# Optimization experiments

Measured on AMD Instinct MI355X. Metric: run time of the kernel, lower is better.

Reference implementation:

```python
import jax, jax.numpy as jnp
import numpy as np

N, E = 50000, 600000
NODE_DIM, EDGE_DIM, MSG_DIM = 128, 64, 128


def setup_inputs() -> dict:
    key = jax.random.key(0)
    ks = jax.random.split(key, 8)
    s = 0.05
    return {
        "node_features": jax.random.normal(ks[0], (N, NODE_DIM), jnp.float32),
        "edge_features": jax.random.normal(ks[1], (E, EDGE_DIM), jnp.float32),
        "edge_index": jax.random.randint(ks[2], (2, E), 0, N, jnp.int32),
        "We1": jax.random.normal(ks[3], (2 * NODE_DIM + EDGE_DIM, 32), jnp.float32) * s,
        "be1": jnp.zeros((32,), jnp.float32),
        "We2": jax.random.normal(ks[4], (32, MSG_DIM), jnp.float32) * s,
        "be2": jnp.zeros((MSG_DIM,), jnp.float32),
        "Wn1": jax.random.normal(ks[5], (NODE_DIM + MSG_DIM, 64), jnp.float32) * s,
        "bn1": jnp.zeros((64,), jnp.float32),
        "Wn2": jax.random.normal(ks[6], (64, MSG_DIM), jnp.float32) * s,
        "bn2": jnp.zeros((MSG_DIM,), jnp.float32),
    }


def reference(node_features, edge_features, edge_index,
              We1, be1, We2, be2, Wn1, bn1, Wn2, bn2):
    src, dst = edge_index[0], edge_index[1]
    src_f = node_features[src]            # [E, node_dim] gather
    dst_f = node_features[dst]            # [E, node_dim] gather
    # edge message encoder: 2-layer MLP with ReLU
    edge_in = jnp.concatenate([src_f, dst_f, edge_features], axis=1)  # [E, 2*nd+ed]
    h = jax.nn.relu(edge_in @ We1 + be1)
    edge_msg = jax.nn.relu(h @ We2 + be2)  # [E, msg_dim]
    # node message encoder
    node_in = jnp.concatenate([dst_f, edge_msg], axis=1)  # [E, nd+md]
    h2 = jax.nn.relu(node_in @ Wn1 + bn1)
    node_msg = jax.nn.relu(h2 @ Wn2 + bn2)  # [E, msg_dim]
    # scatter-sum over destination nodes (replaces the O(N) python loop)
    agg = jax.ops.segment_sum(node_msg, dst, num_segments=node_features.shape[0])
    return node_features + agg
```

## Files before the change

kernel.cpp:

```cpp
#include <hip/hip_runtime.h>
#include <hip/hip_bf16.h>

constexpr int N_NODES = 50000;
constexpr int N_EDGES = 600000;
constexpr int ND = 128;
constexpr int ED = 64;
constexpr int MD = 128;
constexpr int H1 = 32;
constexpr int H2 = 64;

typedef __attribute__((ext_vector_type(8))) short short8;
typedef __attribute__((ext_vector_type(4))) float f32x4;
typedef __attribute__((ext_vector_type(4))) unsigned int uint32x4;

#define MFMA16(a, b, c) __builtin_amdgcn_mfma_f32_16x16x32_bf16((a), (b), (c), 0, 0, 0)

constexpr int COUNTS_PAD = 53248;
constexpr size_t WS_SLOTREC = 0;
constexpr size_t WS_PRE     = WS_SLOTREC + (size_t)N_EDGES * 16;
constexpr size_t WS_POS     = WS_PRE + (size_t)N_NODES * 128 * 2;
constexpr size_t WS_COUNTS  = WS_POS + (size_t)N_EDGES * 4;
constexpr size_t WS_OFFSETS = WS_COUNTS + (size_t)COUNTS_PAD * 4;
constexpr size_t WS_WFE     = ((WS_OFFSETS + (size_t)(N_NODES + 1) * 4 + 15) / 16) * 16;
constexpr size_t WS_WFN     = WS_WFE + (size_t)44 * 64 * 16;
constexpr size_t WS_END     = WS_WFN + (size_t)32 * 64 * 16;

__device__ inline float bflo(unsigned u) { return __uint_as_float(u << 16); }
__device__ inline float bfhi(unsigned u) { return __uint_as_float(u & 0xffff0000u); }
__device__ inline short f2bf(float f) {
    __hip_bfloat16 h = __float2bfloat16(f);
    return *reinterpret_cast<short*>(&h);
}
__device__ inline unsigned pkbf(float a, float b) {
    unsigned r;
    asm("v_cvt_pk_bf16_f32 %0, %1, %2" : "=v"(r) : "v"(a), "v"(b));
    return r;
}
__device__ inline unsigned prelu(float a, float b) {
    return pkbf(fmaxf(a, 0.0f), fmaxf(b, 0.0f));
}
__device__ inline short8 pack8(unsigned w0, unsigned w1, unsigned w2, unsigned w3) {
    uint32x4 t{w0, w1, w2, w3};
    return __builtin_bit_cast(short8, t);
}

__device__ inline int hperm(int kt, int kq) {
    return (kt * 2 + ((kq >> 2) & 1)) * 16 + ((kq >> 3) & 3) * 4 + (kq & 3);
}

__global__ __launch_bounds__(256) void wprep(
    const float* __restrict__ We1, const float* __restrict__ We2,
    const float* __restrict__ Wn1, const float* __restrict__ Wn2,
    short8* __restrict__ wfE, short8* __restrict__ wfN)
{
    const int g = blockIdx.x * 256 + threadIdx.x;
    const int lane = g & 63;
    const int f = g >> 6;
    const int m16 = lane & 15, quad = lane >> 4;
    short v[8];
    if (f < 44) {
        #pragma unroll
        for (int j = 0; j < 8; ++j) {
            const int kq = quad * 8 + j;
            float s;
            if (f < 4) {
                const int kt = f >> 1, mt = f & 1;
                s = We1[(size_t)(2 * ND + kt * 32 + kq) * H1 + mt * 16 + m16];
            } else if (f < 12) {
                const int mt = f - 4;
                s = We2[(size_t)hperm(0, kq) * MD + mt * 16 + m16];
            } else if (f < 28) {
                const int ff = f - 12, kt = ff >> 2, mt = ff & 3;
                s = Wn1[(size_t)(ND + hperm(kt, kq)) * H2 + mt * 16 + m16];
            } else {
                const int ff = f - 28, kt = ff >> 3, mt = ff & 7;
                s = Wn2[(size_t)hperm(kt, kq) * MD + mt * 16 + m16];
            }
            v[j] = f2bf(s);
        }
        wfE[g] = short8{v[0], v[1], v[2], v[3], v[4], v[5], v[6], v[7]};
    } else {
        const int ff = f - 44, kt = ff >> 3, nt = ff & 7;
        const int n = nt * 16 + m16;
        #pragma unroll
        for (int j = 0; j < 8; ++j) {
            const int k = kt * 32 + quad * 8 + j;
            float s;
            if (n < 32)      s = We1[(size_t)k * H1 + n];
            else if (n < 64) s = We1[(size_t)(ND + k) * H1 + (n - 32)];
            else             s = Wn1[(size_t)k * H2 + (n - 64)];
            v[j] = f2bf(s);
        }
        wfN[(size_t)(f - 44) * 64 + lane] = short8{v[0], v[1], v[2], v[3], v[4], v[5], v[6], v[7]};
    }
}

__global__ __launch_bounds__(256) void hist_pos(const int* __restrict__ eidx,
                                                int* __restrict__ counts,
                                                int* __restrict__ pos) {
    const int e = blockIdx.x * 256 + threadIdx.x;
    if (e < N_EDGES) pos[e] = atomicAdd(&counts[eidx[N_EDGES + e]], 1);
}

__global__ __launch_bounds__(1024) void scan_kernel(const int* __restrict__ counts,
                                                    int* __restrict__ offsets) {
    constexpr int T = 1024;
    const int tid = threadIdx.x;
    const int base = tid * 52;
    int4 v[13];
    int s = 0;
    const int4* pc = (const int4*)(counts + base);
    #pragma unroll
    for (int i = 0; i < 13; ++i) {
        v[i] = pc[i];
        s += v[i].x + v[i].y + v[i].z + v[i].w;
    }
    __shared__ int sm[T];
    sm[tid] = s;
    __syncthreads();
    for (int off = 1; off < T; off <<= 1) {
        const int t = (tid >= off) ? sm[tid - off] : 0;
        __syncthreads();
        sm[tid] += t;
        __syncthreads();
    }
    int run = sm[tid] - s;
    #pragma unroll
    for (int i = 0; i < 13; ++i) {
        const int idx = base + i * 4;
        if (idx     <= N_NODES) offsets[idx]     = run;  run += v[i].x;
        if (idx + 1 <= N_NODES) offsets[idx + 1] = run;  run += v[i].y;
        if (idx + 2 <= N_NODES) offsets[idx + 2] = run;  run += v[i].z;
        if (idx + 3 <= N_NODES) offsets[idx + 3] = run;  run += v[i].w;
    }
}

__global__ __launch_bounds__(256) void invert(const int* __restrict__ eidx,
                                              const int* __restrict__ pos,
                                              const int* __restrict__ offsets,
                                              uint4* __restrict__ slotrec) {
    const int e = blockIdx.x * 256 + threadIdx.x;
    if (e < N_EDGES) {
        const int src = eidx[e];
        const int dst = eidx[N_EDGES + e];
        const int slot = offsets[dst] + pos[e];
        slotrec[slot] = uint4{(unsigned)e, (unsigned)src, (unsigned)dst, 0u};
    }
}

__global__ __launch_bounds__(256) void node_pre_mfma(
    const float* __restrict__ nf, const short8* __restrict__ wfN,
    unsigned short* __restrict__ pre, float* __restrict__ out)
{
    __shared__ short ost[4][2048];
    const int tid = threadIdx.x;
    const int w = tid >> 6, lane = tid & 63;
    const int m16 = lane & 15, quad = lane >> 4;
    const int n0 = blockIdx.x * 64 + w * 16;

    {
        const int nbase = blockIdx.x * 64;
        const int nrem = min(64, N_NODES - nbase);
        const float4* s4 = (const float4*)(nf + (size_t)nbase * ND);
        float4* d4 = (float4*)(out + (size_t)nbase * ND);
        const int tot = nrem * (ND / 4);
        for (int i = tid; i < tot; i += 256) d4[i] = s4[i];
    }

    short8 a[4];
    #pragma unroll
    for (int kt = 0; kt < 4; ++kt) {
        const int node = min(n0 + m16, N_NODES - 1);
        const float* pn = nf + (size_t)node * ND + kt * 32 + quad * 8;
        const float4 f0 = *(const float4*)pn;
        const float4 f1 = *(const float4*)(pn + 4);
        a[kt] = pack8(pkbf(f0.x, f0.y), pkbf(f0.z, f0.w),
                      pkbf(f1.x, f1.y), pkbf(f1.z, f1.w));
    }
    f32x4 acc[8];
    #pragma unroll
    for (int nt = 0; nt < 8; ++nt) acc[nt] = f32x4{0.f, 0.f, 0.f, 0.f};
    #pragma unroll
    for (int kt = 0; kt < 4; ++kt) {
        #pragma unroll
        for (int nt = 0; nt < 8; ++nt)
            acc[nt] = MFMA16(a[kt], wfN[(size_t)(kt * 8 + nt) * 64 + lane], acc[nt]);
    }
    short* o = &ost[w][0];
    #pragma unroll
    for (int nt = 0; nt < 8; ++nt)
        #pragma unroll
        for (int r = 0; r < 4; ++r)
            o[(quad * 4 + r) * 128 + nt * 16 + m16] = f2bf(acc[nt][r]);
    asm volatile("s_waitcnt lgkmcnt(0)" ::: "memory");
    #pragma unroll
    for (int i = 0; i < 4; ++i) {
        const int row = i * 4 + quad;
        const int node = n0 + row;
        if (node < N_NODES) {
            const uint4 v = ((const uint4*)(o + row * 128))[m16];
            *((uint4*)(pre + (size_t)node * 128) + m16) = v;
        }
    }
}

__global__ __launch_bounds__(256, 4) void edge_mfma(
    const float* __restrict__ ef, const uint4* __restrict__ slotrec,
    const unsigned short* __restrict__ pre,
    const int* __restrict__ offsets, const short8* __restrict__ wfE,
    const float* __restrict__ be1, const float* __restrict__ be2,
    const float* __restrict__ bn1, const float* __restrict__ bn2,
    const float* __restrict__ nf, float* __restrict__ out)
{
    constexpr int TE = 128;
    __shared__ __align__(16) char sws[4][9216];
    __shared__ int dstlds[TE];

    const int tid = threadIdx.x;
    const int s0 = blockIdx.x * TE;
    const bool hasB = (s0 + 64) < N_EDGES;
    const int w = tid >> 6, lane = tid & 63;
    const int m16 = lane & 15, q = lane >> 4;
    const int er0 = w * 16;
    char* swsb = &sws[w][0];

    float4 efv[2][4];
    {
        const uint4 rA = slotrec[s0 + er0 + m16];
        const float* pe = ef + (size_t)rA.x * ED + q * 8;
        efv[0][0] = *(const float4*)pe;
        efv[0][1] = *(const float4*)(pe + 4);
        efv[0][2] = *(const float4*)(pe + 32);
        efv[0][3] = *(const float4*)(pe + 36);
        if (hasB) {
            const uint4 rB = slotrec[s0 + 64 + er0 + m16];
            const float* pe2 = ef + (size_t)rB.x * ED + q * 8;
            efv[1][0] = *(const float4*)pe2;
            efv[1][1] = *(const float4*)(pe2 + 4);
            efv[1][2] = *(const float4*)(pe2 + 32);
            efv[1][3] = *(const float4*)(pe2 + 36);
        }
    }

    {
        const int et = tid >> 2, p4 = tid & 3;
        const uint4 rA = slotrec[s0 + et];
        const int srcA = (int)rA.y;
        const int dstA = (int)rA.z;
        const uint4* paA = (const uint4*)(pre + (size_t)srcA * 128);
        const uint4* pdA = (const uint4*)(pre + (size_t)dstA * 128);
        const uint4 uaA = paA[p4];
        const uint4 udA = pdA[4 + p4];
        const uint4 s0A = pdA[8 + 2 * p4];
        const uint4 s1A = pdA[9 + 2 * p4];

        uint4 uaB, udB, s0B, s1B;
        int dstB = 0;
        if (hasB) {
            const uint4 rB = slotrec[s0 + 64 + et];
            const int srcB = (int)rB.y;
            dstB = (int)rB.z;
            const uint4* paB = (const uint4*)(pre + (size_t)srcB * 128);
            const uint4* pdB = (const uint4*)(pre + (size_t)dstB * 128);
            uaB = paB[p4];
            udB = pdB[4 + p4];
            s0B = pdB[8 + 2 * p4];
            s1B = pdB[9 + 2 * p4];
        }
        const float4 b0 = ((const float4*)be1)[2 * p4];
        const float4 b1 = ((const float4*)be1)[2 * p4 + 1];

        char* wbase = &sws[et >> 4][0] + (et & 15) * 144;
        {
            float4 r0, r1;
            r0.x = bflo(uaA.x) + bflo(udA.x) + b0.x;
            r0.y = bfhi(uaA.x) + bfhi(udA.x) + b0.y;
            r0.z = bflo(uaA.y) + bflo(udA.y) + b0.z;
            r0.w = bfhi(uaA.y) + bfhi(udA.y) + b0.w;
            r1.x = bflo(uaA.z) + bflo(udA.z) + b1.x;
            r1.y = bfhi(uaA.z) + bfhi(udA.z) + b1.y;
            r1.z = bflo(uaA.w) + bflo(udA.w) + b1.z;
            r1.w = bfhi(uaA.w) + bfhi(udA.w) + b1.w;
            *(float4*)(wbase + p4 * 32) = r0;
            *(float4*)(wbase + p4 * 32 + 16) = r1;
            *(uint4*)(wbase + 2304 + p4 * 32) = s0A;
            *(uint4*)(wbase + 2304 + p4 * 32 + 16) = s1A;
            if (p4 == 3) dstlds[et] = dstA;
        }
        if (hasB) {
            float4 r0, r1;
            r0.x = bflo(uaB.x) + bflo(udB.x) + b0.x;
            r0.y = bfhi(uaB.x) + bfhi(udB.x) + b0.y;
            r0.z = bflo(uaB.y) + bflo(udB.y) + b0.z;
            r0.w = bfhi(uaB.y) + bfhi(udB.y) + b0.w;
            r1.x = bflo(uaB.z) + bflo(udB.z) + b1.x;
            r1.y = bfhi(uaB.z) + bfhi(udB.z) + b1.y;
            r1.z = bflo(uaB.w) + bflo(udB.w) + b1.z;
            r1.w = bfhi(uaB.w) + bfhi(udB.w) + b1.w;
            *(float4*)(wbase + 4608 + p4 * 32) = r0;
            *(float4*)(wbase + 4608 + p4 * 32 + 16) = r1;
            *(uint4*)(wbase + 4608 + 2304 + p4 * 32) = s0B;
            *(uint4*)(wbase + 4608 + 2304 + p4 * 32 + 16) = s1B;
            if (p4 == 3) dstlds[64 + et] = dstB;
        }
    }
    asm volatile("s_waitcnt lgkmcnt(0)" ::: "memory");

    short8 aef[2][2];
    #pragma unroll
    for (int t = 0; t < 2; ++t) {
        aef[t][0] = pack8(pkbf(efv[t][0].x, efv[t][0].y), pkbf(efv[t][0].z, efv[t][0].w),
                          pkbf(efv[t][1].x, efv[t][1].y), pkbf(efv[t][1].z, efv[t][1].w));
        aef[t][1] = pack8(pkbf(efv[t][2].x, efv[t][2].y), pkbf(efv[t][2].z, efv[t][2].w),
                          pkbf(efv[t][3].x, efv[t][3].y), pkbf(efv[t][3].z, efv[t][3].w));
    }

    f32x4 acc1[2][2];
    #pragma unroll
    for (int t = 0; t < 2; ++t)
        #pragma unroll
        for (int mt = 0; mt < 2; ++mt)
            acc1[t][mt] = *(const f32x4*)(swsb + t * 4608 + m16 * 144 + mt * 64 + q * 16);
    #pragma unroll
    for (int kt = 0; kt < 2; ++kt)
        #pragma unroll
        for (int mt = 0; mt < 2; ++mt) {
            const short8 wf = wfE[(size_t)(kt * 2 + mt) * 64 + lane];
            acc1[0][mt] = MFMA16(wf, aef[0][kt], acc1[0][mt]);
            acc1[1][mt] = MFMA16(wf, aef[1][kt], acc1[1][mt]);
        }

    short8 b2[2];
    #pragma unroll
    for (int t = 0; t < 2; ++t)
        b2[t] = pack8(prelu(acc1[t][0][0], acc1[t][0][1]), prelu(acc1[t][0][2], acc1[t][0][3]),
                      prelu(acc1[t][1][0], acc1[t][1][1]), prelu(acc1[t][1][2], acc1[t][1][3]));

    f32x4 acc2[2][8];
    #pragma unroll
    for (int mt = 0; mt < 8; ++mt) {
        const float4 bb = *(const float4*)(be2 + mt * 16 + q * 4);
        const short8 wf = wfE[(size_t)(4 + mt) * 64 + lane];
        acc2[0][mt] = f32x4{bb.x, bb.y, bb.z, bb.w};
        acc2[1][mt] = acc2[0][mt];
        acc2[0][mt] = MFMA16(wf, b2[0], acc2[0][mt]);
        acc2[1][mt] = MFMA16(wf, b2[1], acc2[1][mt]);
    }
    short8 b3[2][4];
    #pragma unroll
    for (int t = 0; t < 2; ++t)
        #pragma unroll
        for (int kt = 0; kt < 4; ++kt)
            b3[t][kt] = pack8(prelu(acc2[t][2 * kt][0], acc2[t][2 * kt][1]),
                              prelu(acc2[t][2 * kt][2], acc2[t][2 * kt][3]),
                              prelu(acc2[t][2 * kt + 1][0], acc2[t][2 * kt + 1][1]),
                              prelu(acc2[t][2 * kt + 1][2], acc2[t][2 * kt + 1][3]));

    f32x4 acc3[2][4];
    #pragma unroll
    for (int mt = 0; mt < 4; ++mt) {
        const float4 bb = *(const float4*)(bn1 + mt * 16 + q * 4);
        #pragma unroll
        for (int t = 0; t < 2; ++t) {
            const uint2 ua = *(const uint2*)(swsb + t * 4608 + 2304 + m16 * 144 + mt * 32 + q * 8);
            acc3[t][mt] = f32x4{bb.x + bflo(ua.x), bb.y + bfhi(ua.x),
                                bb.z + bflo(ua.y), bb.w + bfhi(ua.y)};
        }
    }
    #pragma unroll
    for (int kt = 0; kt < 4; ++kt)
        #pragma unroll
        for (int mt = 0; mt < 4; ++mt) {
            const short8 wf = wfE[(size_t)(12 + kt * 4 + mt) * 64 + lane];
            acc3[0][mt] = MFMA16(wf, b3[0][kt], acc3[0][mt]);
            acc3[1][mt] = MFMA16(wf, b3[1][kt], acc3[1][mt]);
        }
    short8 b4[2][2];
    #pragma unroll
    for (int t = 0; t < 2; ++t)
        #pragma unroll
        for (int kt = 0; kt < 2; ++kt)
            b4[t][kt] = pack8(prelu(acc3[t][2 * kt][0], acc3[t][2 * kt][1]),
                              prelu(acc3[t][2 * kt][2], acc3[t][2 * kt][3]),
                              prelu(acc3[t][2 * kt + 1][0], acc3[t][2 * kt + 1][1]),
                              prelu(acc3[t][2 * kt + 1][2], acc3[t][2 * kt + 1][3]));

    f32x4 acc4[2][8];
    #pragma unroll
    for (int mt = 0; mt < 8; ++mt) {
        const float4 bb = *(const float4*)(bn2 + mt * 16 + q * 4);
        acc4[0][mt] = f32x4{bb.x, bb.y, bb.z, bb.w};
        acc4[1][mt] = acc4[0][mt];
    }
    #pragma unroll
    for (int kt = 0; kt < 2; ++kt)
        #pragma unroll
        for (int mt = 0; mt < 8; ++mt) {
            const short8 wf = wfE[(size_t)(28 + kt * 8 + mt) * 64 + lane];
            acc4[0][mt] = MFMA16(wf, b4[0][kt], acc4[0][mt]);
            acc4[1][mt] = MFMA16(wf, b4[1][kt], acc4[1][mt]);
        }

    #pragma unroll
    for (int t = 0; t < 2; ++t)
        #pragma unroll
        for (int mt = 0; mt < 8; ++mt) {
            uint2 wv;
            wv.x = prelu(acc4[t][mt][0], acc4[t][mt][1]);
            wv.y = prelu(acc4[t][mt][2], acc4[t][mt][3]);
            *(uint2*)(swsb + t * 4608 + m16 * 272 + mt * 32 + q * 8) = wv;
        }
    __syncthreads();

    const int nsl = hasB ? 128 : 64;
    const int send = s0 + nsl;
    const int dstlo = dstlds[0];
    const int dsthi = dstlds[nsl - 1];
    const int g = tid >> 4, j = tid & 15;
    for (int n = dstlo + g; n <= dsthi; n += 16) {
        const int beg = offsets[n];
        const int end = offsets[n + 1];
        const int lo = max(beg, s0);
        const int hi = min(end, send);
        if (lo >= hi) continue;
        float s[8] = {0.f, 0.f, 0.f, 0.f, 0.f, 0.f, 0.f, 0.f};
        for (int sl = lo - s0; sl < hi - s0; ++sl) {
            const int ww = (sl >> 4) & 3;
            const int tt = sl >> 6;
            const int mm = sl & 15;
            const uint4 u = *(const uint4*)(&sws[ww][0] + tt * 4608 + mm * 272 + j * 16);
            s[0] += bflo(u.x); s[1] += bfhi(u.x);
            s[2] += bflo(u.y); s[3] += bfhi(u.y);
            s[4] += bflo(u.z); s[5] += bfhi(u.z);
            s[6] += bflo(u.w); s[7] += bfhi(u.w);
        }
        if (beg >= s0 && end <= send) {
            const float4* pn = (const float4*)(nf + (size_t)n * ND) + j * 2;
            const float4 n0 = pn[0];
            const float4 n1 = pn[1];
            float4 o0{s[0] + n0.x, s[1] + n0.y, s[2] + n0.z, s[3] + n0.w};
            float4 o1{s[4] + n1.x, s[5] + n1.y, s[6] + n1.z, s[7] + n1.w};
            float4* po = (float4*)(out + (size_t)n * ND) + j * 2;
            po[0] = o0;
            po[1] = o1;
        } else {
            float* po = out + (size_t)n * ND + j * 8;
            #pragma unroll
            for (int r = 0; r < 8; ++r) atomicAdd(po + r, s[r]);
        }
    }
}

extern "C" void kernel_launch(void* const* d_in, const int* in_sizes, int n_in,
                              void* d_out, int out_size, void* d_ws, size_t ws_size,
                              hipStream_t stream) {
    const float* nf  = (const float*)d_in[0];
    const float* ef  = (const float*)d_in[1];
    const int*  eidx = (const int*)d_in[2];
    const float* We1 = (const float*)d_in[3];
    const float* be1 = (const float*)d_in[4];
    const float* We2 = (const float*)d_in[5];
    const float* be2 = (const float*)d_in[6];
    const float* Wn1 = (const float*)d_in[7];
    const float* bn1 = (const float*)d_in[8];
    const float* Wn2 = (const float*)d_in[9];
    const float* bn2 = (const float*)d_in[10];
    float* out = (float*)d_out;

    char* ws = (char*)d_ws;
    uint4* slotrec       = (uint4*)(ws + WS_SLOTREC);
    unsigned short* pre  = (unsigned short*)(ws + WS_PRE);
    int* pos             = (int*)(ws + WS_POS);
    int* counts          = (int*)(ws + WS_COUNTS);
    int* offsets         = (int*)(ws + WS_OFFSETS);
    short8* wfE          = (short8*)(ws + WS_WFE);
    short8* wfN          = (short8*)(ws + WS_WFN);
    (void)ws_size; (void)WS_END;

    hipMemsetAsync(counts, 0, (size_t)COUNTS_PAD * 4, stream);
    wprep<<<19, 256, 0, stream>>>(We1, We2, Wn1, Wn2, wfE, wfN);
    hist_pos<<<(N_EDGES + 255) / 256, 256, 0, stream>>>(eidx, counts, pos);
    scan_kernel<<<1, 1024, 0, stream>>>(counts, offsets);
    invert<<<(N_EDGES + 255) / 256, 256, 0, stream>>>(eidx, pos, offsets, slotrec);
    node_pre_mfma<<<(N_NODES + 63) / 64, 256, 0, stream>>>(nf, wfN, pre, out);
    edge_mfma<<<(N_EDGES + 127) / 128, 256, 0, stream>>>(
        ef, slotrec, pre, offsets, wfE, be1, be2, bn1, bn2, nf, out);
}
```

Baseline: 408.4 us.

## Fuse counts zeroing and slot inversion into other kernels, prefetch MFMA weights

Zeroing of the counts buffer moves into extra blocks of the weight-prep kernel, replacing the separate memset. The invert kernel is folded into node_pre_mfma, where each block handles 768 edges. Weight fragments are loaded into registers ahead of the MFMA loops in both node_pre and edge_mfma, and edge_mfma's occupancy hint drops from 4 to 3 waves to make room for those registers. This saves two launches and hides weight-load latency, at the cost of fewer resident waves per SIMD in the edge kernel.

Result: no change. 411.2 us (+0.7%).

```diff
diff --git a/kernel.cpp b/kernel.cpp
--- a/kernel.cpp
+++ b/kernel.cpp
@@ -51,8 +51,14 @@
 __global__ __launch_bounds__(256) void wprep(
     const float* __restrict__ We1, const float* __restrict__ We2,
     const float* __restrict__ Wn1, const float* __restrict__ Wn2,
-    short8* __restrict__ wfE, short8* __restrict__ wfN)
+    short8* __restrict__ wfE, short8* __restrict__ wfN,
+    int* __restrict__ counts)
 {
+    if (blockIdx.x >= 19) {
+        const int idx = (blockIdx.x - 19) * 256 + threadIdx.x;
+        ((int4*)counts)[idx] = int4{0, 0, 0, 0};
+        return;
+    }
     const int g = blockIdx.x * 256 + threadIdx.x;
     const int lane = g & 63;
     const int f = g >> 6;
@@ -135,21 +141,10 @@
     }
 }
 
-__global__ __launch_bounds__(256) void invert(const int* __restrict__ eidx,
-                                              const int* __restrict__ pos,
-                                              const int* __restrict__ offsets,
-                                              uint4* __restrict__ slotrec) {
-    const int e = blockIdx.x * 256 + threadIdx.x;
-    if (e < N_EDGES) {
-        const int src = eidx[e];
-        const int dst = eidx[N_EDGES + e];
-        const int slot = offsets[dst] + pos[e];
-        slotrec[slot] = uint4{(unsigned)e, (unsigned)src, (unsigned)dst, 0u};
-    }
-}
-
 __global__ __launch_bounds__(256) void node_pre_mfma(
     const float* __restrict__ nf, const short8* __restrict__ wfN,
+    const int* __restrict__ eidx, const int* __restrict__ pos,
+    const int* __restrict__ offsets, uint4* __restrict__ slotrec,
     unsigned short* __restrict__ pre, float* __restrict__ out)
 {
     __shared__ short ost[4][2048];
@@ -159,6 +154,20 @@
     const int n0 = blockIdx.x * 64 + w * 16;
 
     {
+        const int ebase = blockIdx.x * 768;
+        #pragma unroll
+        for (int i = 0; i < 3; ++i) {
+            const int e = ebase + i * 256 + tid;
+            if (e < N_EDGES) {
+                const int src = eidx[e];
+                const int dst = eidx[N_EDGES + e];
+                const int slot = offsets[dst] + pos[e];
+                slotrec[slot] = uint4{(unsigned)e, (unsigned)src, (unsigned)dst, 0u};
+            }
+        }
+    }
+
+    {
         const int nbase = blockIdx.x * 64;
         const int nrem = min(64, N_NODES - nbase);
         const float4* s4 = (const float4*)(nf + (size_t)nbase * ND);
@@ -180,11 +189,19 @@
     f32x4 acc[8];
     #pragma unroll
     for (int nt = 0; nt < 8; ++nt) acc[nt] = f32x4{0.f, 0.f, 0.f, 0.f};
+    short8 wbuf[2][8];
+    #pragma unroll
+    for (int i = 0; i < 8; ++i) wbuf[0][i] = wfN[(size_t)i * 64 + lane];
     #pragma unroll
     for (int kt = 0; kt < 4; ++kt) {
+        if (kt < 3) {
+            #pragma unroll
+            for (int i = 0; i < 8; ++i)
+                wbuf[(kt + 1) & 1][i] = wfN[(size_t)((kt + 1) * 8 + i) * 64 + lane];
+        }
         #pragma unroll
         for (int nt = 0; nt < 8; ++nt)
-            acc[nt] = MFMA16(a[kt], wfN[(size_t)(kt * 8 + nt) * 64 + lane], acc[nt]);
+            acc[nt] = MFMA16(a[kt], wbuf[kt & 1][nt], acc[nt]);
     }
     short* o = &ost[w][0];
     #pragma unroll
@@ -204,7 +221,7 @@
     }
 }
 
-__global__ __launch_bounds__(256, 4) void edge_mfma(
+__global__ __launch_bounds__(256, 3) void edge_mfma(
     const float* __restrict__ ef, const uint4* __restrict__ slotrec,
     const unsigned short* __restrict__ pre,
     const int* __restrict__ offsets, const short8* __restrict__ wfE,
@@ -241,6 +258,12 @@
             efv[1][3] = *(const float4*)(pe2 + 36);
         }
     }
+
+    short8 wf1[4], wf2[8];
+    #pragma unroll
+    for (int i = 0; i < 4; ++i) wf1[i] = wfE[(size_t)i * 64 + lane];
+    #pragma unroll
+    for (int i = 0; i < 8; ++i) wf2[i] = wfE[(size_t)(4 + i) * 64 + lane];
 
     {
         const int et = tid >> 2, p4 = tid & 3;
@@ -325,10 +348,13 @@
     for (int kt = 0; kt < 2; ++kt)
         #pragma unroll
         for (int mt = 0; mt < 2; ++mt) {
-            const short8 wf = wfE[(size_t)(kt * 2 + mt) * 64 + lane];
-            acc1[0][mt] = MFMA16(wf, aef[0][kt], acc1[0][mt]);
-            acc1[1][mt] = MFMA16(wf, aef[1][kt], acc1[1][mt]);
-        }
+            acc1[0][mt] = MFMA16(wf1[kt * 2 + mt], aef[0][kt], acc1[0][mt]);
+            acc1[1][mt] = MFMA16(wf1[kt * 2 + mt], aef[1][kt], acc1[1][mt]);
+        }
+
+    short8 wf3a[8];
+    #pragma unroll
+    for (int i = 0; i < 8; ++i) wf3a[i] = wfE[(size_t)(12 + i) * 64 + lane];
 
     short8 b2[2];
     #pragma unroll
@@ -340,12 +366,16 @@
     #pragma unroll
     for (int mt = 0; mt < 8; ++mt) {
         const float4 bb = *(const float4*)(be2 + mt * 16 + q * 4);
-        const short8 wf = wfE[(size_t)(4 + mt) * 64 + lane];
         acc2[0][mt] = f32x4{bb.x, bb.y, bb.z, bb.w};
         acc2[1][mt] = acc2[0][mt];
-        acc2[0][mt] = MFMA16(wf, b2[0], acc2[0][mt]);
-        acc2[1][mt] = MFMA16(wf, b2[1], acc2[1][mt]);
-    }
+        acc2[0][mt] = MFMA16(wf2[mt], b2[0], acc2[0][mt]);
+        acc2[1][mt] = MFMA16(wf2[mt], b2[1], acc2[1][mt]);
+    }
+
+    short8 wf3b[8];
+    #pragma unroll
+    for (int i = 0; i < 8; ++i) wf3b[i] = wfE[(size_t)(20 + i) * 64 + lane];
+
     short8 b3[2][4];
     #pragma unroll
     for (int t = 0; t < 2; ++t)
@@ -368,12 +398,21 @@
         }
     }
     #pragma unroll
-    for (int kt = 0; kt < 4; ++kt)
+    for (int kt = 0; kt < 2; ++kt)
         #pragma unroll
         for (int mt = 0; mt < 4; ++mt) {
-            const short8 wf = wfE[(size_t)(12 + kt * 4 + mt) * 64 + lane];
-            acc3[0][mt] = MFMA16(wf, b3[0][kt], acc3[0][mt]);
-            acc3[1][mt] = MFMA16(wf, b3[1][kt], acc3[1][mt]);
+            acc3[0][mt] = MFMA16(wf3a[kt * 4 + mt], b3[0][kt], acc3[0][mt]);
+            acc3[1][mt] = MFMA16(wf3a[kt * 4 + mt], b3[1][kt], acc3[1][mt]);
+        }
+    short8 wf4a[8];
+    #pragma unroll
+    for (int i = 0; i < 8; ++i) wf4a[i] = wfE[(size_t)(28 + i) * 64 + lane];
+    #pragma unroll
+    for (int kt = 2; kt < 4; ++kt)
+        #pragma unroll
+        for (int mt = 0; mt < 4; ++mt) {
+            acc3[0][mt] = MFMA16(wf3b[(kt - 2) * 4 + mt], b3[0][kt], acc3[0][mt]);
+            acc3[1][mt] = MFMA16(wf3b[(kt - 2) * 4 + mt], b3[1][kt], acc3[1][mt]);
         }
     short8 b4[2][2];
     #pragma unroll
@@ -385,6 +424,10 @@
                               prelu(acc3[t][2 * kt + 1][0], acc3[t][2 * kt + 1][1]),
                               prelu(acc3[t][2 * kt + 1][2], acc3[t][2 * kt + 1][3]));
 
+    short8 wf4b[8];
+    #pragma unroll
+    for (int i = 0; i < 8; ++i) wf4b[i] = wfE[(size_t)(36 + i) * 64 + lane];
+
     f32x4 acc4[2][8];
     #pragma unroll
     for (int mt = 0; mt < 8; ++mt) {
@@ -393,13 +436,15 @@
         acc4[1][mt] = acc4[0][mt];
     }
     #pragma unroll
-    for (int kt = 0; kt < 2; ++kt)
-        #pragma unroll
-        for (int mt = 0; mt < 8; ++mt) {
-            const short8 wf = wfE[(size_t)(28 + kt * 8 + mt) * 64 + lane];
-            acc4[0][mt] = MFMA16(wf, b4[0][kt], acc4[0][mt]);
-            acc4[1][mt] = MFMA16(wf, b4[1][kt], acc4[1][mt]);
-        }
+    for (int mt = 0; mt < 8; ++mt) {
+        acc4[0][mt] = MFMA16(wf4a[mt], b4[0][0], acc4[0][mt]);
+        acc4[1][mt] = MFMA16(wf4a[mt], b4[1][0], acc4[1][mt]);
+    }
+    #pragma unroll
+    for (int mt = 0; mt < 8; ++mt) {
+        acc4[0][mt] = MFMA16(wf4b[mt], b4[0][1], acc4[0][mt]);
+        acc4[1][mt] = MFMA16(wf4b[mt], b4[1][1], acc4[1][mt]);
+    }
 
     #pragma unroll
     for (int t = 0; t < 2; ++t)
@@ -477,12 +522,11 @@
     short8* wfN          = (short8*)(ws + WS_WFN);
     (void)ws_size; (void)WS_END;
 
-    hipMemsetAsync(counts, 0, (size_t)COUNTS_PAD * 4, stream);
-    wprep<<<19, 256, 0, stream>>>(We1, We2, Wn1, Wn2, wfE, wfN);
+    wprep<<<71, 256, 0, stream>>>(We1, We2, Wn1, Wn2, wfE, wfN, counts);
     hist_pos<<<(N_EDGES + 255) / 256, 256, 0, stream>>>(eidx, counts, pos);
     scan_kernel<<<1, 1024, 0, stream>>>(counts, offsets);
-    invert<<<(N_EDGES + 255) / 256, 256, 0, stream>>>(eidx, pos, offsets, slotrec);
-    node_pre_mfma<<<(N_NODES + 63) / 64, 256, 0, stream>>>(nf, wfN, pre, out);
+    node_pre_mfma<<<(N_NODES + 63) / 64, 256, 0, stream>>>(
+        nf, wfN, eidx, pos, offsets, slotrec, pre, out);
     edge_mfma<<<(N_EDGES + 127) / 128, 256, 0, stream>>>(
         ef, slotrec, pre, offsets, wfE, be1, be2, bn1, bn2, nf, out);
 }
```
